# Kernel tuning notes

Hardware: AMD Instinct MI355X
Metric: run time of the kernel (lower is better)

Reference implementation:

```python
import jax, jax.numpy as jnp
import numpy as np

B, NC, NF, H = 16384, 64, 128, 64
F32_EPS = float(np.finfo(np.float32).eps)


def _cast_rays(t_vals, origins, directions):
    return origins[..., None, :] + t_vals[..., None] * directions[..., None, :]


def _mlp(x, w1, b1, w2, b2, wr, br, wd, bd):
    h = jax.nn.relu(x @ w1 + b1)
    h = jax.nn.relu(h @ w2 + b2)
    rgb = jax.nn.sigmoid(h @ wr + br)          # rgb_activation = Sigmoid, rgb_padding = 0
    density = jax.nn.relu(h @ wd + bd)         # density_activation = ReLU, density_bias = 0
    return rgb, density


def _piecewise_constant_pdf(bins, weights, num_samples):
    # bins: [B, n_bins+1], weights: [B, n_bins]
    eps = 1e-5
    ws = jnp.sum(weights, axis=-1, keepdims=True)
    pad = jnp.maximum(eps - ws, 0.0)
    weights = weights + pad / weights.shape[-1]
    ws = ws + pad
    pdf = weights / ws
    cdf = jnp.minimum(jnp.cumsum(pdf[..., :-1], axis=-1), 1.0)
    cdf = jnp.concatenate([jnp.zeros_like(cdf[..., :1]), cdf, jnp.ones_like(cdf[..., :1])], -1)
    u = jnp.linspace(0.0, 1.0 - F32_EPS, num_samples, dtype=cdf.dtype)
    u = jnp.broadcast_to(u, cdf.shape[:-1] + (num_samples,))
    mask = u[..., None, :] >= cdf[..., :, None]   # [B, n_bins+1, num_samples]

    def find_interval(x):
        x0 = jnp.max(jnp.where(mask, x[..., None], x[..., :1, None]), axis=-2)
        x1 = jnp.min(jnp.where(~mask, x[..., None], x[..., -1:, None]), axis=-2)
        return x0, x1

    bins_g0, bins_g1 = find_interval(bins)
    cdf_g0, cdf_g1 = find_interval(cdf)
    t = jnp.clip(jnp.nan_to_num((u - cdf_g0) / (cdf_g1 - cdf_g0), nan=0.0), 0.0, 1.0)
    samples = bins_g0 + t * (bins_g1 - bins_g0)
    return jax.lax.stop_gradient(samples)       # samples.detach() in original


def _volumetric_rendering(rgb, density, t_vals, dirs, color_bkgd):
    t_dists = jnp.concatenate([t_vals[..., 1:] - t_vals[..., :-1], jnp.full_like(t_vals[..., :1], 1e10)], -1)
    delta = t_dists * jnp.linalg.norm(dirs, axis=-1, keepdims=True)
    dd = density[..., 0] * delta
    alpha = 1.0 - jnp.exp(-dd)
    trans = jnp.exp(-jnp.concatenate([jnp.zeros_like(dd[..., :1]), jnp.cumsum(dd[..., :-1], axis=-1)], -1))
    weights = alpha * trans
    comp_rgb = jnp.sum(weights[..., None] * rgb, axis=-2)
    acc = jnp.sum(weights, axis=-1)
    depth = jnp.sum(weights * t_vals, axis=-1)  # note: torch code returns depth (disp computation is dead)
    comp_rgb = comp_rgb + color_bkgd * (1.0 - acc[..., None])
    return comp_rgb, depth, acc, weights


def _forward(origins, directions, near, far, color_bkgd,
             w1_c, b1_c, w2_c, b2_c, wrgb_c, brgb_c, wd_c, bd_c,
             w1_f, b1_f, w2_f, b2_f, wrgb_f, brgb_f, wd_f, bd_f):
    # ----- level 0: stratified (non-randomized) coarse sampling -----
    t = jnp.linspace(0.0, 1.0, NC)
    t_vals = near * (1.0 - t) + far * t                    # [B, NC]
    samples = _cast_rays(t_vals, origins, directions)      # [B, NC, 3]
    rgb, density = _mlp(samples, w1_c, b1_c, w2_c, b2_c, wrgb_c, brgb_c, wd_c, bd_c)
    comp0, depth0, acc0, w = _volumetric_rendering(rgb, density, t_vals, directions, color_bkgd)
    pts0 = jnp.sum(w[..., None] * samples[0], axis=-2)     # faithful quirk: original uses samples[0]
    # ----- level 1: hierarchical inverse-CDF sampling merged with coarse -----
    bins = 0.5 * (t_vals[..., 1:] + t_vals[..., :-1])      # [B, NC-1]
    z_samples = _piecewise_constant_pdf(bins, w[..., 1:-1], NF)
    z_vals = jnp.sort(jnp.concatenate([t_vals, z_samples], -1), axis=-1)  # [B, NC+NF]
    samples_f = _cast_rays(z_vals, origins, directions)    # [B, NC+NF, 3]
    rgb_f, density_f = _mlp(samples_f, w1_f, b1_f, w2_f, b2_f, wrgb_f, brgb_f, wd_f, bd_f)
    comp1, depth1, acc1, w_f = _volumetric_rendering(rgb_f, density_f, z_vals, directions, color_bkgd)
    pts1 = jnp.sum(w_f[..., None] * samples_f[0], axis=-2)
    return jnp.concatenate([comp0, depth0[:, None], acc0[:, None], pts0,
                            comp1, depth1[:, None], acc1[:, None], pts1], -1)  # [B, 16]


def setup_inputs():
    key = jax.random.key(0)
    ks = jax.random.split(key, 5)

    def mlp_params(k):
        k1, k2, k3, k4 = jax.random.split(k, 4)
        return (jax.random.normal(k1, (3, H)) * 0.5, jnp.zeros((H,)),
                jax.random.normal(k2, (H, H)) * 0.2, jnp.zeros((H,)),
                jax.random.normal(k3, (H, 3)) * 0.2, jnp.zeros((3,)),
                jax.random.normal(k4, (H, 1)) * 0.2, jnp.zeros((1,)))

    w1_c, b1_c, w2_c, b2_c, wrgb_c, brgb_c, wd_c, bd_c = mlp_params(ks[0])
    w1_f, b1_f, w2_f, b2_f, wrgb_f, brgb_f, wd_f, bd_f = mlp_params(ks[1])
    dirs = jax.random.normal(ks[2], (B, 3))
    dirs = dirs / jnp.linalg.norm(dirs, axis=-1, keepdims=True)
    return {
        'origins': jax.random.normal(ks[3], (B, 3)),
        'directions': dirs,
        'near': jnp.full((B, 1), 2.0),
        'far': jnp.full((B, 1), 6.0),
        'color_bkgd': jax.random.uniform(ks[4], (3,)),
        'w1_c': w1_c, 'b1_c': b1_c, 'w2_c': w2_c, 'b2_c': b2_c,
        'wrgb_c': wrgb_c, 'brgb_c': brgb_c, 'wd_c': wd_c, 'bd_c': bd_c,
        'w1_f': w1_f, 'b1_f': b1_f, 'w2_f': w2_f, 'b2_f': b2_f,
        'wrgb_f': wrgb_f, 'brgb_f': brgb_f, 'wd_f': wd_f, 'bd_f': bd_f,
    }


def reference(origins, directions, near, far, color_bkgd,
              w1_c, b1_c, w2_c, b2_c, wrgb_c, brgb_c, wd_c, bd_c,
              w1_f, b1_f, w2_f, b2_f, wrgb_f, brgb_f, wd_f, bd_f):
    return _forward(origins, directions, near, far, color_bkgd,
                    w1_c, b1_c, w2_c, b2_c, wrgb_c, brgb_c, wd_c, bd_c,
                    w1_f, b1_f, w2_f, b2_f, wrgb_f, brgb_f, wd_f, bd_f)
```

## Files before the change

### kernel.cpp

```cpp
#include <hip/hip_runtime.h>
#include <math.h>

#define NRAYS 16384
#define NC    64
#define NF    128
#define NZ    192
#define H     64

typedef __attribute__((ext_vector_type(8))) short bf16x8;
typedef __attribute__((ext_vector_type(4))) float f32x4;
typedef __attribute__((ext_vector_type(4))) int   i32x4;

__device__ __forceinline__ float wave_incl_scan(float v, int lane) {
#pragma unroll
  for (int off = 1; off < 64; off <<= 1) {
    float n = __shfl_up(v, off);
    v = (lane >= off) ? v + n : v;
  }
  return v;
}

__device__ __forceinline__ float wave_incl_max_scan(float v, int lane) {
#pragma unroll
  for (int off = 1; off < 64; off <<= 1) {
    float n = __shfl_up(v, off);
    v = (lane >= off) ? fmaxf(v, n) : v;
  }
  return v;
}

__device__ __forceinline__ float wave_sum(float v) {
#pragma unroll
  for (int off = 32; off > 0; off >>= 1) v += __shfl_xor(v, off);
  return v;
}

__device__ __forceinline__ void split_bf16(float f, short& hi, short& lo) {
  unsigned u = __float_as_uint(f);
  hi = (short)(u >> 16);
  float rem = f - __uint_as_float(u & 0xFFFF0000u);
  lo = (short)(__float_as_uint(rem) >> 16);
}

__device__ __forceinline__ float fsig(float x) {
  return __builtin_amdgcn_rcpf(1.f + __expf(-x));
}

struct __align__(16) WLds {
  float W1b[H][4];
};

struct MfmaW {
  bf16x8 Bhi[2][4], Blo[2][4];
  float  hbown;
};

__device__ __forceinline__ void load_mfma_weights(
    int lane,
    const float* __restrict__ w2,
    const float* __restrict__ br, const float* __restrict__ bd,
    MfmaW& M)
{
  const int quad = lane >> 4, n16 = lane & 15;
#pragma unroll
  for (int kt = 0; kt < 2; ++kt) {
#pragma unroll
    for (int jt = 0; jt < 4; ++jt) {
#pragma unroll
      for (int j = 0; j < 8; ++j) {
        const int k = kt*32 + quad*8 + j;
        short hi, lo;
        split_bf16(w2[k*H + jt*16 + n16], hi, lo);
        M.Bhi[kt][jt][j] = hi; M.Blo[kt][jt][j] = lo;
      }
    }
  }
  const int c = n16 & 3;
  M.hbown = (c == 0) ? br[0] : (c == 1) ? br[1] : (c == 2) ? br[2] : bd[0];
}

__device__ __forceinline__ void mlp_mfma_batch(
    int lane, const float2* __restrict__ AB,
    const float* __restrict__ zsrc, const MfmaW& M,
    const float (*__restrict__ sHW)[4], const float* __restrict__ sB2,
    float* __restrict__ R)
{
  const int quad = lane >> 4, n16 = lane & 15;
  float b2q[4];
#pragma unroll
  for (int jt = 0; jt < 4; ++jt) b2q[jt] = sB2[jt*16 + n16];
#pragma unroll 1
  for (int mt = 0; mt < 4; ++mt) {
    const float z = zsrc[mt*16 + n16];
    f32x4 C[4];
#pragma unroll
    for (int jt = 0; jt < 4; ++jt)
      C[jt] = (f32x4){b2q[jt], b2q[jt], b2q[jt], b2q[jt]};
#pragma unroll
    for (int kt = 0; kt < 2; ++kt) {
      const float4* abp = (const float4*)(AB + kt*32 + quad*8);
      i32x4 hip, lop;
#pragma unroll
      for (int j2 = 0; j2 < 4; ++j2) {
        const float4 p = abp[j2];
        const float h0 = fmaxf(fmaf(z, p.y, p.x), 0.f);
        const float h1 = fmaxf(fmaf(z, p.w, p.z), 0.f);
        const unsigned u0 = __float_as_uint(h0), u1 = __float_as_uint(h1);
        hip[j2] = (int)((u0 >> 16) | (u1 & 0xFFFF0000u));
        const float r0 = h0 - __uint_as_float(u0 & 0xFFFF0000u);
        const float r1 = h1 - __uint_as_float(u1 & 0xFFFF0000u);
        lop[j2] = (int)((__float_as_uint(r0) >> 16) |
                        (__float_as_uint(r1) & 0xFFFF0000u));
      }
      union { i32x4 i; bf16x8 h; } uh, ul;
      uh.i = hip; ul.i = lop;
#pragma unroll
      for (int jt = 0; jt < 4; ++jt) {
        C[jt] = __builtin_amdgcn_mfma_f32_16x16x32_bf16(uh.h, M.Bhi[kt][jt], C[jt], 0, 0, 0);
        C[jt] = __builtin_amdgcn_mfma_f32_16x16x32_bf16(ul.h, M.Bhi[kt][jt], C[jt], 0, 0, 0);
        C[jt] = __builtin_amdgcn_mfma_f32_16x16x32_bf16(uh.h, M.Blo[kt][jt], C[jt], 0, 0, 0);
      }
    }
    float P[16];
#pragma unroll
    for (int i = 0; i < 16; ++i) P[i] = 0.f;
#pragma unroll
    for (int jt = 0; jt < 4; ++jt) {
      const float4 hwv = *(const float4*)(&sHW[jt*16 + n16][0]);
#pragma unroll
      for (int r = 0; r < 4; ++r) {
        const float h2v = fmaxf(C[jt][r], 0.f);
        P[r*4 + 0] = fmaf(h2v, hwv.x, P[r*4 + 0]);
        P[r*4 + 1] = fmaf(h2v, hwv.y, P[r*4 + 1]);
        P[r*4 + 2] = fmaf(h2v, hwv.z, P[r*4 + 2]);
        P[r*4 + 3] = fmaf(h2v, hwv.w, P[r*4 + 3]);
      }
    }
    const bool b0 = (n16 & 1), b1 = (n16 & 2), b2_ = (n16 & 4), b3 = (n16 & 8);
    float Q[8];
#pragma unroll
    for (int s = 0; s < 8; ++s) {
      const float give = b0 ? P[2*s] : P[2*s+1];
      const float keep = b0 ? P[2*s+1] : P[2*s];
      Q[s] = keep + __shfl_xor(give, 1);
    }
    float U[4];
#pragma unroll
    for (int t = 0; t < 4; ++t) {
      const float give = b1 ? Q[2*t] : Q[2*t+1];
      const float keep = b1 ? Q[2*t+1] : Q[2*t];
      U[t] = keep + __shfl_xor(give, 2);
    }
    float V[2];
#pragma unroll
    for (int u = 0; u < 2; ++u) {
      const float give = b2_ ? U[2*u] : U[2*u+1];
      const float keep = b2_ ? U[2*u+1] : U[2*u];
      V[u] = keep + __shfl_xor(give, 4);
    }
    {
      const float give = b3 ? V[0] : V[1];
      const float keep = b3 ? V[1] : V[0];
      const float total = keep + __shfl_xor(give, 8);
      R[mt*64 + lane] = total + M.hbown;
    }
  }
  __builtin_amdgcn_wave_barrier();
}

__device__ __forceinline__ void coarse_pass(
    int ray, int lane,
    const float* __restrict__ origins, const float* __restrict__ dirs,
    const float* __restrict__ nearp, const float* __restrict__ farp,
    const float* __restrict__ bkgd,
    const WLds& W, const MfmaW& M,
    const float (*__restrict__ sHW)[4], const float* __restrict__ sB2,
    float* __restrict__ R, float2* __restrict__ sAB,
    float* __restrict__ sT, float* __restrict__ sBins,
    float* __restrict__ sCdf, float* __restrict__ sZs,
    float* __restrict__ zdst, bool emit, float* __restrict__ out)
{
  const float nearv = nearp[ray];
  const float farv  = farp[ray];
  const float ox = origins[ray*3+0], oy = origins[ray*3+1], oz = origins[ray*3+2];
  const float dx = dirs[ray*3+0],    dy = dirs[ray*3+1],    dz = dirs[ray*3+2];

  {
    const float4 wv = *(const float4*)(&W.W1b[lane][0]);
    const float a = fmaf(ox, wv.x, fmaf(oy, wv.y, fmaf(oz, wv.z, wv.w)));
    const float b = fmaf(dx, wv.x, fmaf(dy, wv.y, dz * wv.z));
    sAB[lane] = (float2){a, b};
  }

  const float u_i  = (float)lane / 63.0f;
  const float u_n  = (float)(lane + 1) / 63.0f;
  const float tv    = nearv * (1.f - u_i) + farv * u_i;
  const float tnext = nearv * (1.f - u_n) + farv * u_n;

  sT[lane] = tv;
  if (lane < NC-1) sBins[lane] = 0.5f * (tv + tnext);
  zdst[lane] = 0.f; zdst[lane+64] = 0.f; zdst[lane+128] = 0.f;
  __builtin_amdgcn_wave_barrier();

  mlp_mfma_batch(lane, sAB, sT, M, sHW, sB2, R);
  const float4 rr = *(const float4*)(&R[lane*4]);
  const float rgb0 = fsig(rr.x), rgb1 = fsig(rr.y), rgb2 = fsig(rr.z);
  const float dens = fmaxf(rr.w, 0.f);

  const float dnorm = sqrtf(dx*dx + dy*dy + dz*dz);
  const float tdist = (lane == NC-1) ? 1e10f : (tnext - tv);
  const float dd    = fminf(dens * (tdist * dnorm), 1e4f);
  const float incl  = wave_incl_scan(dd, lane);
  const float excl  = incl - dd;
  const float alpha = 1.f - expf(-dd);
  const float trans = expf(-excl);
  const float w     = alpha * trans;

  if (emit) {
    const float near0 = nearp[0], far0 = farp[0];
    const float t0v   = near0 * (1.f - u_i) + far0 * u_i;
    const float s_w   = wave_sum(w);
    const float s_wt  = wave_sum(w * tv);
    const float s_c0  = wave_sum(w * rgb0);
    const float s_c1  = wave_sum(w * rgb1);
    const float s_c2  = wave_sum(w * rgb2);
    const float s_wt0 = wave_sum(w * t0v);
    if (lane == 0) {
      const float bk0 = bkgd[0], bk1 = bkgd[1], bk2 = bkgd[2];
      const float o0x = origins[0], o0y = origins[1], o0z = origins[2];
      const float d0x = dirs[0],    d0y = dirs[1],    d0z = dirs[2];
      const float oma = 1.f - s_w;
      float* o = out + (size_t)ray * 16;
      o[0] = s_c0 + bk0 * oma;
      o[1] = s_c1 + bk1 * oma;
      o[2] = s_c2 + bk2 * oma;
      o[3] = s_wt;
      o[4] = s_w;
      o[5] = s_w * o0x + s_wt0 * d0x;
      o[6] = s_w * o0y + s_wt0 * d0y;
      o[7] = s_w * o0z + s_wt0 * d0z;
    }
  }

  const float wnext = __shfl_down(w, 1);
  const float pw = (lane < NC-2) ? wnext : 0.f;
  const float ws_sum = wave_sum(pw);
  const float pad = fmaxf(1e-5f - ws_sum, 0.f);
  const float wsp = ws_sum + pad;
  const float pdf = (lane < NC-2) ? (pw + pad * (1.f/62.f)) / wsp : 0.f;
  float ip  = wave_incl_scan(pdf, lane);
  ip = wave_incl_max_scan(ip, lane);
  if (lane < 61)  sCdf[lane+1] = fminf(ip, 1.f);
  if (lane == 61) sCdf[0]  = 0.f;
  if (lane == 62) sCdf[62] = 1.f;
  __builtin_amdgcn_wave_barrier();

  const float ustep = (1.0f - 1.1920929e-07f) / 127.0f;
#pragma unroll
  for (int r = 0; r < 2; ++r) {
    const int k = lane + 64*r;
    const float u = k * ustep;
    int lo = 0, hi = 61;
    while (lo < hi) {
      const int mid = (lo + hi + 1) >> 1;
      if (sCdf[mid] <= u) lo = mid; else hi = mid - 1;
    }
    const int J = lo;
    const float cg0 = sCdf[J],  cg1 = sCdf[J+1];
    const float bg0 = sBins[J], bg1 = sBins[J+1];
    const float denom = cg1 - cg0;
    const float num   = u - cg0;
    float tt;
    if (denom > 0.f) tt = fminf(fmaxf(num / denom, 0.f), 1.f);
    else             tt = (num > 0.f) ? 1.f : 0.f;
    sZs[k] = fmaf(tt, bg1 - bg0, bg0);
  }
  __builtin_amdgcn_wave_barrier();

  {
    int l = 0, r = NF;
    while (l < r) { const int m = (l + r) >> 1; if (sZs[m] < tv) l = m + 1; else r = m; }
    zdst[lane + l] = tv;
  }
#pragma unroll
  for (int r2 = 0; r2 < 2; ++r2) {
    const int k = lane + 64*r2;
    const float z = sZs[k];
    int l = 0, r = NC;
    while (l < r) { const int m = (l + r) >> 1; if (sT[m] <= z) l = m + 1; else r = m; }
    zdst[k + l] = z;
  }
  __builtin_amdgcn_wave_barrier();
}

__global__ __launch_bounds__(64) void nerf_z0_kernel(
    const float* __restrict__ origins, const float* __restrict__ dirs,
    const float* __restrict__ nearp, const float* __restrict__ farp,
    const float* __restrict__ w1c, const float* __restrict__ b1c,
    const float* __restrict__ w2c, const float* __restrict__ b2c,
    const float* __restrict__ wrc, const float* __restrict__ brc,
    const float* __restrict__ wdc, const float* __restrict__ bdc,
    float* __restrict__ gz0)
{
  __shared__ WLds sW;
  __shared__ float sHW[H][4];
  __shared__ float sB2[H];
  __shared__ float sT[NC], sBins[NC], sCdf[NC], sZs[NF], sZv0[NZ];
  __shared__ float sR[256];
  __shared__ __align__(16) float2 sAB[H];

  const int lane = threadIdx.x;
  {
    const int k = lane;
    sW.W1b[k][0] = w1c[0*H + k];
    sW.W1b[k][1] = w1c[1*H + k];
    sW.W1b[k][2] = w1c[2*H + k];
    sW.W1b[k][3] = b1c[k];
    sHW[k][0] = wrc[k*3 + 0];
    sHW[k][1] = wrc[k*3 + 1];
    sHW[k][2] = wrc[k*3 + 2];
    sHW[k][3] = wdc[k];
    sB2[k]    = b2c[k];
  }
  __syncthreads();

  MfmaW Mc;
  load_mfma_weights(lane, w2c, brc, bdc, Mc);

  coarse_pass(0, lane, origins, dirs, nearp, farp, nullptr,
              sW, Mc, sHW, sB2, sR, sAB, sT, sBins, sCdf, sZs, sZv0,
              false, nullptr);

#pragma unroll
  for (int s = 0; s < 3; ++s) gz0[lane + 64*s] = sZv0[lane + 64*s];
}

__global__ __launch_bounds__(256) void nerf_fused_kernel(
    const float* __restrict__ origins, const float* __restrict__ dirs,
    const float* __restrict__ nearp, const float* __restrict__ farp,
    const float* __restrict__ bkgd,
    const float* __restrict__ w1c, const float* __restrict__ b1c,
    const float* __restrict__ w2c, const float* __restrict__ b2c,
    const float* __restrict__ wrc, const float* __restrict__ brc,
    const float* __restrict__ wdc, const float* __restrict__ bdc,
    const float* __restrict__ w1f, const float* __restrict__ b1f,
    const float* __restrict__ w2f, const float* __restrict__ b2f_,
    const float* __restrict__ wrf, const float* __restrict__ brf,
    const float* __restrict__ wdf, const float* __restrict__ bdf,
    const float* __restrict__ gz0, float* __restrict__ out)
{
  __shared__ WLds sWc, sWf;
  __shared__ float sHWc[H][4], sHWf[H][4];
  __shared__ float sB2c[H], sB2f[H];
  __shared__ float sT[4][NC];
  __shared__ float sBins[4][NC];
  __shared__ float sCdf[4][NC];
  __shared__ float sZs[4][NF];
  __shared__ float sZv[4][NZ];
  __shared__ float sZv0[NZ];
  __shared__ float sR[4][3*256];
  __shared__ __align__(16) float2 sAB[4][H];

  const int tid  = threadIdx.x;
  const int wv   = tid >> 6;
  const int lane = tid & 63;
  const int ray  = blockIdx.x * 4 + wv;

  if (tid < 64) {
    const int k = tid;
    sWc.W1b[k][0] = w1c[0*H + k];
    sWc.W1b[k][1] = w1c[1*H + k];
    sWc.W1b[k][2] = w1c[2*H + k];
    sWc.W1b[k][3] = b1c[k];
    sHWc[k][0] = wrc[k*3+0]; sHWc[k][1] = wrc[k*3+1];
    sHWc[k][2] = wrc[k*3+2]; sHWc[k][3] = wdc[k];
    sB2c[k] = b2c[k];
  } else if (tid < 128) {
    const int k = tid - 64;
    sWf.W1b[k][0] = w1f[0*H + k];
    sWf.W1b[k][1] = w1f[1*H + k];
    sWf.W1b[k][2] = w1f[2*H + k];
    sWf.W1b[k][3] = b1f[k];
    sHWf[k][0] = wrf[k*3+0]; sHWf[k][1] = wrf[k*3+1];
    sHWf[k][2] = wrf[k*3+2]; sHWf[k][3] = wdf[k];
    sB2f[k] = b2f_[k];
  }
  if (tid < NZ) sZv0[tid] = gz0[tid];
  __syncthreads();

  float* R = sR[wv];
  float2* ABw = &sAB[wv][0];

  {
    MfmaW Mc;
    load_mfma_weights(lane, w2c, brc, bdc, Mc);
    coarse_pass(ray, lane, origins, dirs, nearp, farp, bkgd,
                sWc, Mc, sHWc, sB2c, R, ABw,
                sT[wv], sBins[wv], sCdf[wv], sZs[wv], sZv[wv], true, out);
  }

  MfmaW Mf;
  load_mfma_weights(lane, w2f, brf, bdf, Mf);

  const float ox = origins[ray*3+0], oy = origins[ray*3+1], oz = origins[ray*3+2];
  const float dx = dirs[ray*3+0],    dy = dirs[ray*3+1],    dz = dirs[ray*3+2];
  const float dnorm = sqrtf(dx*dx + dy*dy + dz*dz);

  {
    const float4 wvv = *(const float4*)(&sWf.W1b[lane][0]);
    const float a = fmaf(ox, wvv.x, fmaf(oy, wvv.y, fmaf(oz, wvv.z, wvv.w)));
    const float b = fmaf(dx, wvv.x, fmaf(dy, wvv.y, dz * wvv.z));
    ABw[lane] = (float2){a, b};
  }
  __builtin_amdgcn_wave_barrier();

#pragma unroll
  for (int s = 0; s < 3; ++s)
    mlp_mfma_batch(lane, ABw, &sZv[wv][64*s], Mf, sHWf, sB2f, R + s*256);

  float dd[3];
#pragma unroll
  for (int s = 0; s < 3; ++s) {
    const int i = lane + 64*s;
    const float dens = fmaxf(R[s*256 + lane*4 + 3], 0.f);
    const float zcv = sZv[wv][i];
    const float znv = (i < NZ-1) ? sZv[wv][i+1] : 0.f;
    const float td = (i == NZ-1) ? 1e10f : fmaxf(znv - zcv, 0.f);
    dd[s] = fminf(dens * (td * dnorm), 1e4f);
  }

  float excl[3];
  float offset = 0.f;
#pragma unroll
  for (int s = 0; s < 3; ++s) {
    const float incl = wave_incl_scan(dd[s], lane);
    excl[s] = offset + incl - dd[s];
    offset += __shfl(incl, 63);
  }

  float aw = 0.f, awz = 0.f, ac0 = 0.f, ac1 = 0.f, ac2 = 0.f, awz0 = 0.f;
#pragma unroll
  for (int s = 0; s < 3; ++s) {
    const int i = lane + 64*s;
    const float4 rr = *(const float4*)(&R[s*256 + lane*4]);
    const float wgt = (1.f - __expf(-dd[s])) * __expf(-excl[s]);
    aw   += wgt;
    awz  += wgt * sZv[wv][i];
    ac0  += wgt * fsig(rr.x);
    ac1  += wgt * fsig(rr.y);
    ac2  += wgt * fsig(rr.z);
    awz0 += wgt * sZv0[i];
  }
  aw  = wave_sum(aw);  awz = wave_sum(awz); ac0 = wave_sum(ac0);
  ac1 = wave_sum(ac1); ac2 = wave_sum(ac2); awz0 = wave_sum(awz0);

  if (lane == 0) {
    const float bk0 = bkgd[0], bk1 = bkgd[1], bk2 = bkgd[2];
    const float o0x = origins[0], o0y = origins[1], o0z = origins[2];
    const float d0x = dirs[0],    d0y = dirs[1],    d0z = dirs[2];
    const float oma = 1.f - aw;
    float* o = out + (size_t)ray * 16 + 8;
    o[0] = ac0 + bk0 * oma;
    o[1] = ac1 + bk1 * oma;
    o[2] = ac2 + bk2 * oma;
    o[3] = awz;
    o[4] = aw;
    o[5] = aw * o0x + awz0 * d0x;
    o[6] = aw * o0y + awz0 * d0y;
    o[7] = aw * o0z + awz0 * d0z;
  }
}

extern "C" void kernel_launch(void* const* d_in, const int* in_sizes, int n_in,
                              void* d_out, int out_size, void* d_ws, size_t ws_size,
                              hipStream_t stream) {
  const float* origins = (const float*)d_in[0];
  const float* dirs    = (const float*)d_in[1];
  const float* nearp   = (const float*)d_in[2];
  const float* farp    = (const float*)d_in[3];
  const float* bkgd    = (const float*)d_in[4];
  const float* w1c  = (const float*)d_in[5];
  const float* b1c  = (const float*)d_in[6];
  const float* w2c  = (const float*)d_in[7];
  const float* b2c  = (const float*)d_in[8];
  const float* wrc  = (const float*)d_in[9];
  const float* brc  = (const float*)d_in[10];
  const float* wdc  = (const float*)d_in[11];
  const float* bdc  = (const float*)d_in[12];
  const float* w1f  = (const float*)d_in[13];
  const float* b1f  = (const float*)d_in[14];
  const float* w2f  = (const float*)d_in[15];
  const float* b2f_ = (const float*)d_in[16];
  const float* wrf  = (const float*)d_in[17];
  const float* brf  = (const float*)d_in[18];
  const float* wdf  = (const float*)d_in[19];
  const float* bdf  = (const float*)d_in[20];

  float* gz0 = (float*)d_ws;

  nerf_z0_kernel<<<1, 64, 0, stream>>>(
      origins, dirs, nearp, farp,
      w1c, b1c, w2c, b2c, wrc, brc, wdc, bdc, gz0);

  nerf_fused_kernel<<<NRAYS/4, 256, 0, stream>>>(
      origins, dirs, nearp, farp, bkgd,
      w1c, b1c, w2c, b2c, wrc, brc, wdc, bdc,
      w1f, b1f, w2f, b2f_, wrf, brf, wdf, bdf,
      gz0, (float*)d_out);
}
```

Before: 302.9 us.

## Parallelize z0 pre-kernel coarse MLP across four waves

```diff
diff --git a/kernel.cpp b/kernel.cpp
--- a/kernel.cpp
+++ b/kernel.cpp
@@ -77,6 +77,90 @@
   }
   const int c = n16 & 3;
   M.hbown = (c == 0) ? br[0] : (c == 1) ? br[1] : (c == 2) ? br[2] : bd[0];
+}
+
+__device__ __forceinline__ void mlp_mfma_batch_one(
+    int mt, int lane, const float2* __restrict__ AB,
+    const float* __restrict__ zsrc, const MfmaW& M,
+    const float (*__restrict__ sHW)[4], const float* __restrict__ sB2,
+    float* __restrict__ R)
+{
+  const int quad = lane >> 4, n16 = lane & 15;
+  const float z = zsrc[mt*16 + n16];
+  f32x4 C[4];
+#pragma unroll
+  for (int jt = 0; jt < 4; ++jt) {
+    const float b2v = sB2[jt*16 + n16];
+    C[jt] = (f32x4){b2v, b2v, b2v, b2v};
+  }
+#pragma unroll
+  for (int kt = 0; kt < 2; ++kt) {
+    const float4* abp = (const float4*)(AB + kt*32 + quad*8);
+    i32x4 hip, lop;
+#pragma unroll
+    for (int j2 = 0; j2 < 4; ++j2) {
+      const float4 p = abp[j2];
+      const float h0 = fmaxf(fmaf(z, p.y, p.x), 0.f);
+      const float h1 = fmaxf(fmaf(z, p.w, p.z), 0.f);
+      const unsigned u0 = __float_as_uint(h0), u1 = __float_as_uint(h1);
+      hip[j2] = (int)((u0 >> 16) | (u1 & 0xFFFF0000u));
+      const float r0 = h0 - __uint_as_float(u0 & 0xFFFF0000u);
+      const float r1 = h1 - __uint_as_float(u1 & 0xFFFF0000u);
+      lop[j2] = (int)((__float_as_uint(r0) >> 16) |
+                      (__float_as_uint(r1) & 0xFFFF0000u));
+    }
+    union { i32x4 i; bf16x8 h; } uh, ul;
+    uh.i = hip; ul.i = lop;
+#pragma unroll
+    for (int jt = 0; jt < 4; ++jt) {
+      C[jt] = __builtin_amdgcn_mfma_f32_16x16x32_bf16(uh.h, M.Bhi[kt][jt], C[jt], 0, 0, 0);
+      C[jt] = __builtin_amdgcn_mfma_f32_16x16x32_bf16(ul.h, M.Bhi[kt][jt], C[jt], 0, 0, 0);
+      C[jt] = __builtin_amdgcn_mfma_f32_16x16x32_bf16(uh.h, M.Blo[kt][jt], C[jt], 0, 0, 0);
+    }
+  }
+  float P[16];
+#pragma unroll
+  for (int i = 0; i < 16; ++i) P[i] = 0.f;
+#pragma unroll
+  for (int jt = 0; jt < 4; ++jt) {
+    const float4 hwv = *(const float4*)(&sHW[jt*16 + n16][0]);
+#pragma unroll
+    for (int r = 0; r < 4; ++r) {
+      const float h2v = fmaxf(C[jt][r], 0.f);
+      P[r*4 + 0] = fmaf(h2v, hwv.x, P[r*4 + 0]);
+      P[r*4 + 1] = fmaf(h2v, hwv.y, P[r*4 + 1]);
+      P[r*4 + 2] = fmaf(h2v, hwv.z, P[r*4 + 2]);
+      P[r*4 + 3] = fmaf(h2v, hwv.w, P[r*4 + 3]);
+    }
+  }
+  const bool b0 = (n16 & 1), b1 = (n16 & 2), b2_ = (n16 & 4), b3 = (n16 & 8);
+  float Q[8];
+#pragma unroll
+  for (int s = 0; s < 8; ++s) {
+    const float give = b0 ? P[2*s] : P[2*s+1];
+    const float keep = b0 ? P[2*s+1] : P[2*s];
+    Q[s] = keep + __shfl_xor(give, 1);
+  }
+  float U[4];
+#pragma unroll
+  for (int t = 0; t < 4; ++t) {
+    const float give = b1 ? Q[2*t] : Q[2*t+1];
+    const float keep = b1 ? Q[2*t+1] : Q[2*t];
+    U[t] = keep + __shfl_xor(give, 2);
+  }
+  float V[2];
+#pragma unroll
+  for (int u = 0; u < 2; ++u) {
+    const float give = b2_ ? U[2*u] : U[2*u+1];
+    const float keep = b2_ ? U[2*u+1] : U[2*u];
+    V[u] = keep + __shfl_xor(give, 4);
+  }
+  {
+    const float give = b3 ? V[0] : V[1];
+    const float keep = b3 ? V[1] : V[0];
+    const float total = keep + __shfl_xor(give, 8);
+    R[mt*64 + lane] = total + M.hbown;
+  }
 }
 
 __device__ __forceinline__ void mlp_mfma_batch(
@@ -293,7 +377,7 @@
   __builtin_amdgcn_wave_barrier();
 }
 
-__global__ __launch_bounds__(64) void nerf_z0_kernel(
+__global__ __launch_bounds__(256) void nerf_z0_kernel(
     const float* __restrict__ origins, const float* __restrict__ dirs,
     const float* __restrict__ nearp, const float* __restrict__ farp,
     const float* __restrict__ w1c, const float* __restrict__ b1c,
@@ -309,9 +393,12 @@
   __shared__ float sR[256];
   __shared__ __align__(16) float2 sAB[H];
 
-  const int lane = threadIdx.x;
-  {
-    const int k = lane;
+  const int tid  = threadIdx.x;
+  const int wv   = tid >> 6;
+  const int lane = tid & 63;
+
+  if (tid < 64) {
+    const int k = tid;
     sW.W1b[k][0] = w1c[0*H + k];
     sW.W1b[k][1] = w1c[1*H + k];
     sW.W1b[k][2] = w1c[2*H + k];
@@ -322,17 +409,107 @@
     sHW[k][3] = wdc[k];
     sB2[k]    = b2c[k];
   }
-  __syncthreads();
 
   MfmaW Mc;
   load_mfma_weights(lane, w2c, brc, bdc, Mc);
-
-  coarse_pass(0, lane, origins, dirs, nearp, farp, nullptr,
-              sW, Mc, sHW, sB2, sR, sAB, sT, sBins, sCdf, sZs, sZv0,
-              false, nullptr);
-
-#pragma unroll
-  for (int s = 0; s < 3; ++s) gz0[lane + 64*s] = sZv0[lane + 64*s];
+  __syncthreads();
+
+  const float nearv = nearp[0];
+  const float farv  = farp[0];
+
+  if (wv == 0) {
+    const float ox = origins[0], oy = origins[1], oz = origins[2];
+    const float dx = dirs[0],    dy = dirs[1],    dz = dirs[2];
+    const float4 wvv = *(const float4*)(&sW.W1b[lane][0]);
+    const float a = fmaf(ox, wvv.x, fmaf(oy, wvv.y, fmaf(oz, wvv.z, wvv.w)));
+    const float b = fmaf(dx, wvv.x, fmaf(dy, wvv.y, dz * wvv.z));
+    sAB[lane] = (float2){a, b};
+
+    const float u_i  = (float)lane / 63.0f;
+    const float u_n  = (float)(lane + 1) / 63.0f;
+    const float tv    = nearv * (1.f - u_i) + farv * u_i;
+    const float tnext = nearv * (1.f - u_n) + farv * u_n;
+    sT[lane] = tv;
+    if (lane < NC-1) sBins[lane] = 0.5f * (tv + tnext);
+    sZv0[lane] = 0.f; sZv0[lane+64] = 0.f; sZv0[lane+128] = 0.f;
+  }
+  __syncthreads();
+
+  mlp_mfma_batch_one(wv, lane, sAB, sT, Mc, sHW, sB2, sR);
+  __syncthreads();
+
+  if (wv == 0) {
+    const float dx = dirs[0], dy = dirs[1], dz = dirs[2];
+    const float u_i  = (float)lane / 63.0f;
+    const float u_n  = (float)(lane + 1) / 63.0f;
+    const float tv    = nearv * (1.f - u_i) + farv * u_i;
+    const float tnext = nearv * (1.f - u_n) + farv * u_n;
+
+    const float4 rr = *(const float4*)(&sR[lane*4]);
+    const float dens = fmaxf(rr.w, 0.f);
+
+    const float dnorm = sqrtf(dx*dx + dy*dy + dz*dz);
+    const float tdist = (lane == NC-1) ? 1e10f : (tnext - tv);
+    const float dd    = fminf(dens * (tdist * dnorm), 1e4f);
+    const float incl  = wave_incl_scan(dd, lane);
+    const float excl  = incl - dd;
+    const float alpha = 1.f - expf(-dd);
+    const float trans = expf(-excl);
+    const float w     = alpha * trans;
+
+    const float wnext = __shfl_down(w, 1);
+    const float pw = (lane < NC-2) ? wnext : 0.f;
+    const float ws_sum = wave_sum(pw);
+    const float pad = fmaxf(1e-5f - ws_sum, 0.f);
+    const float wsp = ws_sum + pad;
+    const float pdf = (lane < NC-2) ? (pw + pad * (1.f/62.f)) / wsp : 0.f;
+    float ip  = wave_incl_scan(pdf, lane);
+    ip = wave_incl_max_scan(ip, lane);
+    if (lane < 61)  sCdf[lane+1] = fminf(ip, 1.f);
+    if (lane == 61) sCdf[0]  = 0.f;
+    if (lane == 62) sCdf[62] = 1.f;
+    __builtin_amdgcn_wave_barrier();
+
+    const float ustep = (1.0f - 1.1920929e-07f) / 127.0f;
+#pragma unroll
+    for (int r = 0; r < 2; ++r) {
+      const int k = lane + 64*r;
+      const float u = k * ustep;
+      int lo = 0, hi = 61;
+      while (lo < hi) {
+        const int mid = (lo + hi + 1) >> 1;
+        if (sCdf[mid] <= u) lo = mid; else hi = mid - 1;
+      }
+      const int J = lo;
+      const float cg0 = sCdf[J],  cg1 = sCdf[J+1];
+      const float bg0 = sBins[J], bg1 = sBins[J+1];
+      const float denom = cg1 - cg0;
+      const float num   = u - cg0;
+      float tt;
+      if (denom > 0.f) tt = fminf(fmaxf(num / denom, 0.f), 1.f);
+      else             tt = (num > 0.f) ? 1.f : 0.f;
+      sZs[k] = fmaf(tt, bg1 - bg0, bg0);
+    }
+    __builtin_amdgcn_wave_barrier();
+
+    {
+      int l = 0, r = NF;
+      while (l < r) { const int m = (l + r) >> 1; if (sZs[m] < tv) l = m + 1; else r = m; }
+      sZv0[lane + l] = tv;
+    }
+#pragma unroll
+    for (int r2 = 0; r2 < 2; ++r2) {
+      const int k = lane + 64*r2;
+      const float z = sZs[k];
+      int l = 0, r = NC;
+      while (l < r) { const int m = (l + r) >> 1; if (sT[m] <= z) l = m + 1; else r = m; }
+      sZv0[k + l] = z;
+    }
+    __builtin_amdgcn_wave_barrier();
+
+#pragma unroll
+    for (int s = 0; s < 3; ++s) gz0[lane + 64*s] = sZv0[lane + 64*s];
+  }
 }
 
 __global__ __launch_bounds__(256) void nerf_fused_kernel(
@@ -498,7 +675,7 @@
 
   float* gz0 = (float*)d_ws;
 
-  nerf_z0_kernel<<<1, 64, 0, stream>>>(
+  nerf_z0_kernel<<<1, 256, 0, stream>>>(
       origins, dirs, nearp, farp,
       w1c, b1c, w2c, b2c, wrc, brc, wdc, bdc, gz0);
 
```

After: 299.9 us. No clear change (-1.0%).
